# Kernel optimization log

Hardware: AMD Instinct MI355X
Metric: run time of the kernel (lower is better)

Reference implementation:

```python
import jax, jax.numpy as jnp
import numpy as np

B, S, H = 64, 2048, 512
NEG = -1e9

def setup_inputs() -> dict:
    key = jax.random.key(0)
    k1, k2, k3, k4, k5 = jax.random.split(key, 5)
    encoder_outputs = jax.random.normal(k1, (B, S, H), dtype=jnp.float32)
    mask = jax.random.randint(k2, (B, S), 0, 2).astype(bool)
    W = jax.random.normal(k3, (H, H), dtype=jnp.float32) / np.sqrt(H)
    b = jnp.zeros((H,), dtype=jnp.float32)
    v = jax.random.normal(k4, (H,), dtype=jnp.float32)  # context_vector
    return {"encoder_outputs": encoder_outputs, "mask": mask, "W": W, "b": b, "v": v}

def reference(encoder_outputs, mask, W, b, v):
    # u = tanh(x @ W^T + b): [B,S,H]
    u = jnp.tanh(jnp.einsum('bsh,oh->bso', encoder_outputs, W) + b)
    scores = jnp.einsum('bsh,h->bs', u, v)                 # [B,S]
    scores = jnp.where(mask, scores, NEG)
    attn_weights = jax.nn.softmax(scores, axis=1)          # [B,S]
    weighted_output = jnp.einsum('bsh,bs->bh', encoder_outputs, attn_weights)
    return weighted_output, attn_weights
```

## Files before the change

### kernel.cpp

```cpp
#include <hip/hip_runtime.h>
#include <hip/hip_fp16.h>
#include <stdint.h>

#define NEG_ (-1e9f)

typedef _Float16 f16x8 __attribute__((ext_vector_type(8)));
typedef float    f32x4 __attribute__((ext_vector_type(4)));

__device__ __forceinline__ float fast_tanh(float x) {
  float e = __expf(2.0f * x);
  return (e - 1.0f) * __builtin_amdgcn_rcpf(e + 1.0f);
}

__global__ __launch_bounds__(256) void k0_cvt_w(const float* __restrict__ W,
                                                __half* __restrict__ Wws) {
  int g = blockIdx.x * 256 + threadIdx.x;
  int lane = g & 63;
  int seg  = g >> 6;
  int io = seg & 3, ks = (seg >> 2) & 15, w = (seg >> 6) & 3, oc = seg >> 8;
  int o = oc * 256 + w * 64 + io * 16 + (lane & 15);
  int k = ks * 32 + (lane >> 4) * 8;
  const float2* src = (const float2*)(W + (size_t)o * 512 + k);
  __half2 h[4];
#pragma unroll
  for (int j = 0; j < 4; ++j) { float2 f = src[j]; h[j] = __floats2half2_rn(f.x, f.y); }
  uint4 u;
  u.x = *(uint32_t*)&h[0]; u.y = *(uint32_t*)&h[1];
  u.z = *(uint32_t*)&h[2]; u.w = *(uint32_t*)&h[3];
  *(uint4*)(Wws + (size_t)seg * 512 + (size_t)lane * 8) = u;
}

__global__ __launch_bounds__(256, 2) void k1_scores(
    const float* __restrict__ enc, const int* __restrict__ msk,
    const float* __restrict__ bias, const float* __restrict__ ctx,
    const __half* __restrict__ Wws, float* __restrict__ scores) {
  __shared__ __align__(16) __half Xl[64 * 512];

  const int t = threadIdx.x;
  const int w = t >> 6;
  const int lane = t & 63;
  const int quad = lane >> 4;
  const int l15 = lane & 15;
  const size_t mtile = blockIdx.x;

  {
    const float4* Xg = (const float4*)(enc + mtile * (size_t)(64 * 512));
#pragma unroll
    for (int j = 0; j < 16; ++j) {
      int g = j * 256 + t;
      int s = g >> 6, c = g & 63;
      float4 x0 = Xg[s * 128 + 2 * c];
      float4 x1 = Xg[s * 128 + 2 * c + 1];
      __half2 h0 = __floats2half2_rn(x0.x, x0.y);
      __half2 h1 = __floats2half2_rn(x0.z, x0.w);
      __half2 h2 = __floats2half2_rn(x1.x, x1.y);
      __half2 h3 = __floats2half2_rn(x1.z, x1.w);
      uint4 u;
      u.x = *(uint32_t*)&h0; u.y = *(uint32_t*)&h1;
      u.z = *(uint32_t*)&h2; u.w = *(uint32_t*)&h3;
      int pc = c ^ (s & 7);
      *(uint4*)&Xl[s * 512 + pc * 8] = u;
    }
  }
  __syncthreads();

  float sacc[4] = {0.f, 0.f, 0.f, 0.f};

  f16x8 abuf[3][4];
  auto aload = [&](int slot, int iter) {
    int oc = iter >> 4, ks = iter & 15;
    const f16x8* sp = (const f16x8*)(Wws +
        ((size_t)((oc * 4 + w) * 64 + ks * 4) * 512) + (size_t)lane * 8);
#pragma unroll
    for (int io = 0; io < 4; ++io) abuf[slot][io] = sp[io * 64];
  };
  aload(0, 0);
  aload(1, 1);

#pragma unroll
  for (int oc = 0; oc < 2; ++oc) {
    f32x4 acc[4][4];
#pragma unroll
    for (int io = 0; io < 4; ++io)
#pragma unroll
      for (int is = 0; is < 4; ++is) acc[io][is] = (f32x4){0.f, 0.f, 0.f, 0.f};

#pragma unroll
    for (int ks = 0; ks < 16; ++ks) {
      const int iter = oc * 16 + ks;
      if (iter + 2 < 32) aload((iter + 2) % 3, iter + 2);
      const f16x8* acur = abuf[iter % 3];
#pragma unroll
      for (int is = 0; is < 4; ++is) {
        int s = is * 16 + l15;
        const f16x8 bf = *(const f16x8*)&Xl[s * 512 + (((ks * 4 + quad) ^ (s & 7)) << 3)];
#pragma unroll
        for (int io = 0; io < 4; ++io)
          acc[io][is] = __builtin_amdgcn_mfma_f32_16x16x32_f16(acur[io], bf, acc[io][is], 0, 0, 0);
      }
    }

    float ps[4] = {0.f, 0.f, 0.f, 0.f};
#pragma unroll
    for (int io = 0; io < 4; ++io) {
      int ob = oc * 256 + w * 64 + io * 16 + quad * 4;
      float4 b4 = *(const float4*)(bias + ob);
      float4 v4 = *(const float4*)(ctx + ob);
#pragma unroll
      for (int is = 0; is < 4; ++is) {
        const f32x4 a = acc[io][is];
        ps[is] += fast_tanh(a[0] + b4.x) * v4.x + fast_tanh(a[1] + b4.y) * v4.y +
                  fast_tanh(a[2] + b4.z) * v4.z + fast_tanh(a[3] + b4.w) * v4.w;
      }
    }
#pragma unroll
    for (int is = 0; is < 4; ++is) {
      float p = ps[is];
      p += __shfl_xor(p, 16, 64);
      p += __shfl_xor(p, 32, 64);
      sacc[is] += p;
    }
  }

  __syncthreads();
  float* sred = (float*)&Xl[0];
  if (lane < 16) {
#pragma unroll
    for (int is = 0; is < 4; ++is) sred[w * 64 + is * 16 + lane] = sacc[is];
  }
  __syncthreads();
  if (t < 64) {
    float sc = sred[t] + sred[64 + t] + sred[128 + t] + sred[192 + t];
    size_t row = mtile * 64 + t;
    scores[row] = msk[row] ? sc : NEG_;
  }
}

__global__ __launch_bounds__(256) void k2_softmax(float* __restrict__ attn) {
  const int b = blockIdx.x, t = threadIdx.x;
  float* row = attn + (size_t)b * 2048;
  float v[8];
  float mx = -3.4e38f;
#pragma unroll
  for (int i = 0; i < 8; ++i) { v[i] = row[t + 256 * i]; mx = fmaxf(mx, v[i]); }
#pragma unroll
  for (int off = 32; off >= 1; off >>= 1) mx = fmaxf(mx, __shfl_xor(mx, off, 64));
  __shared__ float r1[4], r2[4];
  int w = t >> 6, lane = t & 63;
  if (lane == 0) r1[w] = mx;
  __syncthreads();
  mx = fmaxf(fmaxf(r1[0], r1[1]), fmaxf(r1[2], r1[3]));
  float sum = 0.f;
#pragma unroll
  for (int i = 0; i < 8; ++i) { v[i] = __expf(v[i] - mx); sum += v[i]; }
#pragma unroll
  for (int off = 32; off >= 1; off >>= 1) sum += __shfl_xor(sum, off, 64);
  if (lane == 0) r2[w] = sum;
  __syncthreads();
  sum = r2[0] + r2[1] + r2[2] + r2[3];
  float inv = 1.0f / sum;
#pragma unroll
  for (int i = 0; i < 8; ++i) row[t + 256 * i] = v[i] * inv;
}

__global__ __launch_bounds__(256) void k3_wsum(const float* __restrict__ enc,
                                               const float* __restrict__ attn,
                                               float* __restrict__ out0) {
  const int bb = blockIdx.x >> 5, sc = blockIdx.x & 31, t = threadIdx.x;
  const int r = t >> 7;
  const int c = t & 127;
  __shared__ float a_s[64];
  if (t < 64) a_s[t] = attn[(size_t)bb * 2048 + sc * 64 + t];
  __syncthreads();
  const float4* Xg = (const float4*)(enc + ((size_t)bb * 2048 + (size_t)sc * 64) * 512);
  float4 acc = {0.f, 0.f, 0.f, 0.f};
#pragma unroll 8
  for (int s = r; s < 64; s += 2) {
    float a = a_s[s];
    float4 x = Xg[(size_t)s * 128 + c];
    acc.x = fmaf(a, x.x, acc.x);
    acc.y = fmaf(a, x.y, acc.y);
    acc.z = fmaf(a, x.z, acc.z);
    acc.w = fmaf(a, x.w, acc.w);
  }
  float* op = out0 + (size_t)bb * 512 + c * 4;
  atomicAdd(op + 0, acc.x);
  atomicAdd(op + 1, acc.y);
  atomicAdd(op + 2, acc.z);
  atomicAdd(op + 3, acc.w);
}

extern "C" void kernel_launch(void* const* d_in, const int* in_sizes, int n_in,
                              void* d_out, int out_size, void* d_ws, size_t ws_size,
                              hipStream_t stream) {
  (void)in_sizes; (void)n_in; (void)out_size; (void)ws_size;
  const float* enc  = (const float*)d_in[0];
  const int*   msk  = (const int*)d_in[1];
  const float* W    = (const float*)d_in[2];
  const float* bias = (const float*)d_in[3];
  const float* ctx  = (const float*)d_in[4];
  float* out0 = (float*)d_out;
  float* attn = out0 + 64 * 512;
  __half* Wws = (__half*)d_ws;

  hipMemsetAsync(out0, 0, 64 * 512 * sizeof(float), stream);
  k0_cvt_w<<<128, 256, 0, stream>>>(W, Wws);
  k1_scores<<<2048, 256, 0, stream>>>(enc, msk, bias, ctx, Wws, attn);
  k2_softmax<<<64, 256, 0, stream>>>(attn);
  k3_wsum<<<2048, 256, 0, stream>>>(enc, attn, out0);
}
```

Measured before the change: 532.1 us.

## Prefetch W fragments during X staging, ping-pong A registers, replace atomics with two-pass reduce

In the scores kernel, the first W fragment is now loaded before the X tile is converted into LDS, and the three-slot A-register ring becomes a two-buffer ping-pong with the outer oc loop no longer unrolled. The aim is to hide global W latency and to lower register pressure. The weighted-sum stage now writes per-chunk partial sums to workspace and reduces them in a second kernel. This replaces float atomics and the memset, at the cost of one more launch and an extra write and read of the partials.

New measurement: 600.3 us. +12.8%, slower.

```diff
diff --git a/kernel.cpp b/kernel.cpp
--- a/kernel.cpp
+++ b/kernel.cpp
@@ -43,9 +43,16 @@
   const int l15 = lane & 15;
   const size_t mtile = blockIdx.x;
 
+  const __half* wbase = Wws + (size_t)lane * 8;
+
+  f16x8 aP[4], aQ[4];
+#pragma unroll
+  for (int io = 0; io < 4; ++io)
+    aP[io] = *(const f16x8*)(wbase + (size_t)(w * 64 + io) * 512);
+
   {
     const float4* Xg = (const float4*)(enc + mtile * (size_t)(64 * 512));
-#pragma unroll
+#pragma unroll 8
     for (int j = 0; j < 16; ++j) {
       int g = j * 256 + t;
       int s = g >> 6, c = g & 63;
@@ -66,18 +73,6 @@
 
   float sacc[4] = {0.f, 0.f, 0.f, 0.f};
 
-  f16x8 abuf[3][4];
-  auto aload = [&](int slot, int iter) {
-    int oc = iter >> 4, ks = iter & 15;
-    const f16x8* sp = (const f16x8*)(Wws +
-        ((size_t)((oc * 4 + w) * 64 + ks * 4) * 512) + (size_t)lane * 8);
-#pragma unroll
-    for (int io = 0; io < 4; ++io) abuf[slot][io] = sp[io * 64];
-  };
-  aload(0, 0);
-  aload(1, 1);
-
-#pragma unroll
   for (int oc = 0; oc < 2; ++oc) {
     f32x4 acc[4][4];
 #pragma unroll
@@ -85,18 +80,37 @@
 #pragma unroll
       for (int is = 0; is < 4; ++is) acc[io][is] = (f32x4){0.f, 0.f, 0.f, 0.f};
 
-#pragma unroll
-    for (int ks = 0; ks < 16; ++ks) {
-      const int iter = oc * 16 + ks;
-      if (iter + 2 < 32) aload((iter + 2) % 3, iter + 2);
-      const f16x8* acur = abuf[iter % 3];
-#pragma unroll
-      for (int is = 0; is < 4; ++is) {
-        int s = is * 16 + l15;
-        const f16x8 bf = *(const f16x8*)&Xl[s * 512 + (((ks * 4 + quad) ^ (s & 7)) << 3)];
-#pragma unroll
-        for (int io = 0; io < 4; ++io)
-          acc[io][is] = __builtin_amdgcn_mfma_f32_16x16x32_f16(acur[io], bf, acc[io][is], 0, 0, 0);
+    const int segbase = oc * 256 + w * 64;
+
+#pragma unroll
+    for (int kk = 0; kk < 16; kk += 2) {
+      {
+        const __half* np = wbase + (size_t)(segbase + (kk + 1) * 4) * 512;
+#pragma unroll
+        for (int io = 0; io < 4; ++io) aQ[io] = *(const f16x8*)(np + (size_t)io * 512);
+#pragma unroll
+        for (int is = 0; is < 4; ++is) {
+          int s = is * 16 + l15;
+          const f16x8 bf = *(const f16x8*)&Xl[s * 512 + (((kk * 4 + quad) ^ (s & 7)) << 3)];
+#pragma unroll
+          for (int io = 0; io < 4; ++io)
+            acc[io][is] = __builtin_amdgcn_mfma_f32_16x16x32_f16(aP[io], bf, acc[io][is], 0, 0, 0);
+        }
+      }
+      {
+        int niter = oc * 16 + kk + 2;
+        int nseg = (niter < 32) ? ((niter >> 4) * 256 + w * 64 + (niter & 15) * 4) : 0;
+        const __half* np = wbase + (size_t)nseg * 512;
+#pragma unroll
+        for (int io = 0; io < 4; ++io) aP[io] = *(const f16x8*)(np + (size_t)io * 512);
+#pragma unroll
+        for (int is = 0; is < 4; ++is) {
+          int s = is * 16 + l15;
+          const f16x8 bf = *(const f16x8*)&Xl[s * 512 + ((((kk + 1) * 4 + quad) ^ (s & 7)) << 3)];
+#pragma unroll
+          for (int io = 0; io < 4; ++io)
+            acc[io][is] = __builtin_amdgcn_mfma_f32_16x16x32_f16(aQ[io], bf, acc[io][is], 0, 0, 0);
+        }
       }
     }
 
@@ -163,31 +177,34 @@
   for (int i = 0; i < 8; ++i) row[t + 256 * i] = v[i] * inv;
 }
 
-__global__ __launch_bounds__(256) void k3_wsum(const float* __restrict__ enc,
-                                               const float* __restrict__ attn,
-                                               float* __restrict__ out0) {
+__global__ __launch_bounds__(256) void k3a_wsum(const float* __restrict__ enc,
+                                                const float* __restrict__ attn,
+                                                float* __restrict__ part) {
   const int bb = blockIdx.x >> 5, sc = blockIdx.x & 31, t = threadIdx.x;
-  const int r = t >> 7;
-  const int c = t & 127;
   __shared__ float a_s[64];
   if (t < 64) a_s[t] = attn[(size_t)bb * 2048 + sc * 64 + t];
   __syncthreads();
-  const float4* Xg = (const float4*)(enc + ((size_t)bb * 2048 + (size_t)sc * 64) * 512);
-  float4 acc = {0.f, 0.f, 0.f, 0.f};
+  const float2* Xg = (const float2*)(enc + ((size_t)bb * 2048 + (size_t)sc * 64) * 512) + t;
+  float2 acc = {0.f, 0.f};
 #pragma unroll 8
-  for (int s = r; s < 64; s += 2) {
+  for (int s = 0; s < 64; ++s) {
     float a = a_s[s];
-    float4 x = Xg[(size_t)s * 128 + c];
+    float2 x = Xg[(size_t)s * 256];
     acc.x = fmaf(a, x.x, acc.x);
     acc.y = fmaf(a, x.y, acc.y);
-    acc.z = fmaf(a, x.z, acc.z);
-    acc.w = fmaf(a, x.w, acc.w);
-  }
-  float* op = out0 + (size_t)bb * 512 + c * 4;
-  atomicAdd(op + 0, acc.x);
-  atomicAdd(op + 1, acc.y);
-  atomicAdd(op + 2, acc.z);
-  atomicAdd(op + 3, acc.w);
+  }
+  *(float2*)(part + ((size_t)blockIdx.x * 512) + 2 * t) = acc;
+}
+
+__global__ __launch_bounds__(256) void k3b_reduce(const float* __restrict__ part,
+                                                  float* __restrict__ out0) {
+  const int idx = blockIdx.x * 256 + threadIdx.x;
+  const int b = idx >> 9, h = idx & 511;
+  const float* p = part + (size_t)b * 32 * 512 + h;
+  float s = 0.f;
+#pragma unroll
+  for (int sc = 0; sc < 32; ++sc) s += p[(size_t)sc * 512];
+  out0[idx] = s;
 }
 
 extern "C" void kernel_launch(void* const* d_in, const int* in_sizes, int n_in,
@@ -202,10 +219,11 @@
   float* out0 = (float*)d_out;
   float* attn = out0 + 64 * 512;
   __half* Wws = (__half*)d_ws;
-
-  hipMemsetAsync(out0, 0, 64 * 512 * sizeof(float), stream);
+  float* part = (float*)((char*)d_ws + 512 * 1024);
+
   k0_cvt_w<<<128, 256, 0, stream>>>(W, Wws);
   k1_scores<<<2048, 256, 0, stream>>>(enc, msk, bias, ctx, Wws, attn);
   k2_softmax<<<64, 256, 0, stream>>>(attn);
-  k3_wsum<<<2048, 256, 0, stream>>>(enc, attn, out0);
-}
+  k3a_wsum<<<2048, 256, 0, stream>>>(enc, attn, part);
+  k3b_reduce<<<128, 256, 0, stream>>>(part, out0);
+}
```
